# Kernel tuning notes

Measured on AMD Instinct MI355X. Metric: run time of the kernel, lower is better.

The kernel has to match this reference:

```python
import jax, jax.numpy as jnp
import numpy as np

WS = 8       # window size
NH = 8       # num heads


def _window_partition(x, ws):
    # x: [B, E, H, W] -> [B*Hn*Wn, ws*ws, E]
    B, E, H, W = x.shape
    Hn, Wn = H // ws, W // ws
    x = x.reshape(B, E, Hn, ws, Wn, ws)
    x = x.transpose(0, 2, 4, 3, 5, 1)  # B, Hn, Wn, ws1, ws2, E
    return x.reshape(B * Hn * Wn, ws * ws, E)


def _window_unpartition(x, B, H, W, ws):
    # x: [B*Hn*Wn, ws*ws, E] -> [B, E, H, W]
    Hn, Wn = H // ws, W // ws
    E = x.shape[-1]
    x = x.reshape(B, Hn, Wn, ws, ws, E)
    x = x.transpose(0, 5, 1, 3, 2, 4)  # B, E, Hn, ws1, Wn, ws2
    return x.reshape(B, E, H, W)


def setup_inputs() -> dict:
    key = jax.random.key(0)
    ks = jax.random.split(key, 5)
    B, E, H, W = 8, 512, 64, 64
    s = 1.0 / np.sqrt(E)
    return {
        "q": jax.random.normal(ks[0], (B, E, H, W), jnp.float32),
        "k": jax.random.normal(ks[1], (B, E, H, W), jnp.float32),
        "v": jax.random.normal(ks[2], (B, E, H, W), jnp.float32),
        "in_proj_w": (jax.random.normal(ks[3], (3 * E, E), jnp.float32) * s),
        "in_proj_b": jnp.zeros((3 * E,), jnp.float32),
        "out_proj_w": (jax.random.normal(ks[4], (E, E), jnp.float32) * s),
        "out_proj_b": jnp.zeros((E,), jnp.float32),
    }


def reference(q, k, v, in_proj_w, in_proj_b, out_proj_w, out_proj_b):
    B, E, H, W = q.shape
    ws, nh = WS, NH
    hd = E // nh

    qw = _window_partition(q, ws)  # [N, T, E], N = B*Hn*Wn, T = ws*ws
    kw = _window_partition(k, ws)
    vw = _window_partition(v, ws)

    Wq, Wk, Wv = in_proj_w[:E], in_proj_w[E:2 * E], in_proj_w[2 * E:]
    bq, bk, bv = in_proj_b[:E], in_proj_b[E:2 * E], in_proj_b[2 * E:]

    qp = qw @ Wq.T + bq
    kp = kw @ Wk.T + bk
    vp = vw @ Wv.T + bv

    N, T, _ = qp.shape
    qh = qp.reshape(N, T, nh, hd)
    kh = kp.reshape(N, T, nh, hd)
    vh = vp.reshape(N, T, nh, hd)

    scale = jnp.asarray(1.0 / np.sqrt(hd), qp.dtype)
    attn = jax.nn.softmax(jnp.einsum('nqhd,nkhd->nhqk', qh, kh) * scale, axis=-1)
    o = jnp.einsum('nhqk,nkhd->nqhd', attn, vh).reshape(N, T, E)
    o = o @ out_proj_w.T + out_proj_b

    return _window_unpartition(o, B, H, W, ws)
```

## Files before the change

kernel.cpp:

```cpp
#include <hip/hip_runtime.h>

typedef __attribute__((ext_vector_type(4))) float f32x4;
typedef __attribute__((ext_vector_type(8))) short short8;
typedef __attribute__((ext_vector_type(4))) unsigned uint4v;

#define E_DIM 512
#define HW    4096
#define NT    32768
#define NTE   16777216

__device__ short g_wbf[2048 * E_DIM];

__device__ __forceinline__ short f2bf(float f) {
  union { float f; unsigned u; } v; v.f = f;
  unsigned u = v.u;
  u += 0x7fffu + ((u >> 16) & 1u);
  return (short)(u >> 16);
}
__device__ __forceinline__ unsigned pack_bf2(float lo, float hi) {
  return (unsigned)(unsigned short)f2bf(lo) | ((unsigned)(unsigned short)f2bf(hi) << 16);
}

__device__ __forceinline__ int swzidx(int row, int k) {
  return row * 64 + (k ^ ((row & 7) << 3));
}

__device__ __forceinline__ void chunk_map(int c, int& row, int& kc) {
  const int line = c >> 3;
  const int l = (c & 7) ^ (line & 7);
  row = line * 2 + (l >> 2);
  kc = l & 3;
}
__device__ __forceinline__ int tile_off(int row, int kc) {
  const int line = row >> 1;
  const int phys = (((row & 1) << 2) | kc) ^ (line & 7);
  return line * 64 + phys * 8;
}

#define GLOAD16(g, l) __builtin_amdgcn_global_load_lds( \
    (const __attribute__((address_space(1))) void*)(g), \
    (__attribute__((address_space(3))) void*)(l), 16, 0, 0)

#define WAITVM(N) asm volatile("s_waitcnt vmcnt(" #N ")" ::: "memory")
#define LGKM0()   asm volatile("s_waitcnt lgkmcnt(0)" ::: "memory")
#define FULL_BAR() do { asm volatile("" ::: "memory"); \
  __builtin_amdgcn_s_barrier(); asm volatile("" ::: "memory"); } while (0)

__global__ __launch_bounds__(256) void convert_w(
    const float* __restrict__ w_in, const float* __restrict__ w_out)
{
  const size_t off = ((size_t)blockIdx.x * 256 + threadIdx.x) * 8;
  const float* src = (off < 786432) ? (w_in + off) : (w_out + (off - 786432));
  f32x4 a = *(const f32x4*)src, b = *(const f32x4*)(src + 4);
  short8 s;
#pragma unroll
  for (int j = 0; j < 4; ++j) { s[j] = f2bf(a[j]); s[4 + j] = f2bf(b[j]); }
  *(short8*)&g_wbf[off] = s;
}

__global__ __launch_bounds__(512, 2) void proj_kernel(
    const float* __restrict__ Xq, const float* __restrict__ Xk,
    const float* __restrict__ Xv, const float* __restrict__ Bfull,
    short* __restrict__ Oq, short* __restrict__ Ok, short* __restrict__ Ov)
{
  const int wg  = blockIdx.x;
  const int swz = (wg & 7) * 96 + (wg >> 3);
  const int z = swz >> 8, rr = swz & 255;
  const int e0 = (rr & 1) << 8, tok0 = (rr >> 1) << 8;

  const float* X  = (z == 0) ? Xq : (z == 1) ? Xk : Xv;
  const short* Wz = g_wbf + z * (E_DIM * E_DIM);
  const float* bias = Bfull + z * E_DIM;
  short* O = (z == 0) ? Oq : (z == 1) ? Ok : Ov;

  const int b   = tok0 >> 12;
  const int hw0 = tok0 & (HW - 1);
  const float* Xb = X + (size_t)b * E_DIM * HW + hw0;

  __shared__ unsigned ldsA[2 * 4096];
  __shared__ short    ldsB[3 * 8192];

  const int tid = threadIdx.x, lane = tid & 63, wv = tid >> 6;
  const int wm = wv >> 2, wn = wv & 3;
  const int lr = lane & 15, lg = lane >> 4;

  const int fp  = tid >> 5;
  const int hw8 = (tid & 31) * 8;
  const float* arow0 = Xb + (size_t)(2 * fp) * HW + hw8;
  const int keyw = (fp >> 3) << 4;
  const int aWbase = fp * 256 + (hw8 ^ keyw);

  int r0, k0c, r1, k1c;
  chunk_map(tid, r0, k0c);
  chunk_map(512 + tid, r1, k1c);
  const short* sB0 = Wz + (size_t)(e0 + r0) * E_DIM + k0c * 8;
  const short* sB1 = Wz + (size_t)(e0 + r1) * E_DIM + k1c * 8;
  const int dc0 = (wv * 64) * 8, dc1 = (512 + wv * 64) * 8;

  const int keyr = (lg >> 1) << 4;
  int aoff[8], boff[4];
#pragma unroll
  for (int i = 0; i < 8; ++i)
    aoff[i] = lg * 1024 + ((wm * 128 + i * 16 + lr) ^ keyr);
#pragma unroll
  for (int j = 0; j < 4; ++j) boff[j] = tile_off(wn * 64 + j * 16 + lr, lg);

  f32x4 acc[8][4];
#pragma unroll
  for (int i = 0; i < 8; ++i)
#pragma unroll
    for (int j = 0; j < 4; ++j) acc[i][j] = (f32x4){0.f, 0.f, 0.f, 0.f};

  f32x4 aX[4], aY[4];

#define ISSUE_A(dst, kt) do { \
    const float* ap = arow0 + (size_t)(kt) * (32 * HW); \
    dst[0] = *(const f32x4*)(ap);          dst[1] = *(const f32x4*)(ap + 4); \
    dst[2] = *(const f32x4*)(ap + HW);     dst[3] = *(const f32x4*)(ap + 4 + HW); \
  } while (0)

#define ISSUE_B(slot, kt) do { \
    const int ko2 = (kt) * 32, sb2 = (slot) * 8192; \
    GLOAD16(sB0 + ko2, &ldsB[sb2 + dc0]); \
    GLOAD16(sB1 + ko2, &ldsB[sb2 + dc1]); \
  } while (0)

#define WRITE_A(slot, src) do { \
    unsigned* dA = &ldsA[(slot) * 4096 + aWbase]; \
    uint4v lo_, hi_; \
    _Pragma("unroll") \
    for (int j = 0; j < 4; ++j) { \
      lo_[j] = pack_bf2(src[0][j], src[2][j]); \
      hi_[j] = pack_bf2(src[1][j], src[3][j]); \
    } \
    *(uint4v*)(dA) = lo_; \
    *(uint4v*)(dA + 4) = hi_; \
  } while (0)

#define COMPUTE(aslot, bslot) do { \
    const unsigned* pa = ldsA + (aslot) * 4096; \
    const short*    pb = ldsB + (bslot) * 8192; \
    short8 af[8], bf[4]; \
    _Pragma("unroll") \
    for (int i = 0; i < 8; ++i) { \
      union { unsigned u[4]; short8 s; } av_; \
      av_.u[0] = pa[aoff[i]];       av_.u[1] = pa[aoff[i] + 256]; \
      av_.u[2] = pa[aoff[i] + 512]; av_.u[3] = pa[aoff[i] + 768]; \
      af[i] = av_.s; \
    } \
    _Pragma("unroll") \
    for (int j = 0; j < 4; ++j) bf[j] = *(const short8*)(pb + boff[j]); \
    __builtin_amdgcn_s_setprio(1); \
    _Pragma("unroll") \
    for (int i = 0; i < 8; ++i) \
      _Pragma("unroll") \
      for (int j = 0; j < 4; ++j) \
        acc[i][j] = __builtin_amdgcn_mfma_f32_16x16x32_bf16(af[i], bf[j], acc[i][j], 0, 0, 0); \
    __builtin_amdgcn_s_setprio(0); \
  } while (0)

  ISSUE_B(0, 0); ISSUE_B(1, 1);
  ISSUE_A(aX, 0);
  ISSUE_A(aY, 1);
  WAITVM(4);
  WRITE_A(0, aX);

  ISSUE_A(aX, 2);
  WAITVM(4); LGKM0();
  FULL_BAR();
  ISSUE_B(2, 2);
  WRITE_A(1, aY);
  COMPUTE(0, 0);

  for (int k = 0; k < 6; ++k) {
    const int t = 2 * k + 1;
    ISSUE_A(aY, t + 2);
    WAITVM(6); LGKM0();
    FULL_BAR();
    ISSUE_B((t + 2) % 3, t + 2);
    WRITE_A(0, aX);
    COMPUTE(1, t % 3);
    ISSUE_A(aX, t + 3);
    WAITVM(6); LGKM0();
    FULL_BAR();
    ISSUE_B((t + 3) % 3, t + 3);
    WRITE_A(1, aY);
    COMPUTE(0, (t + 1) % 3);
  }

  ISSUE_A(aY, 15);
  WAITVM(6); LGKM0();
  FULL_BAR();
  ISSUE_B(0, 15);
  WRITE_A(0, aX);
  COMPUTE(1, 1);
  WAITVM(2); LGKM0();
  FULL_BAR();
  WRITE_A(1, aY);
  COMPUTE(0, 2);
  WAITVM(0); LGKM0();
  FULL_BAR();
  COMPUTE(1, 0);

#undef ISSUE_A
#undef ISSUE_B
#undef WRITE_A
#undef COMPUTE

  float bj[4];
#pragma unroll
  for (int j = 0; j < 4; ++j) bj[j] = bias[e0 + wn * 64 + j * 16 + lr];
#pragma unroll
  for (int i = 0; i < 8; ++i) {
#pragma unroll
    for (int r = 0; r < 4; ++r) {
      const int token = tok0 + wm * 128 + i * 16 + lg * 4 + r;
      const int hw = token & (HW - 1);
      const int h = hw >> 6, w = hw & 63;
      const int nwin = ((token >> 12) << 6) + ((h >> 3) << 3) + (w >> 3);
      const int twin = ((h & 7) << 3) + (w & 7);
      short* orow = O + ((size_t)(nwin * 64 + twin) << 9) + e0 + wn * 64 + lr;
#pragma unroll
      for (int j = 0; j < 4; ++j)
        orow[j * 16] = f2bf(acc[i][j][r] + bj[j]);
    }
  }
}

__global__ __launch_bounds__(256) void attn_kernel(
    const short* __restrict__ Qp, const short* __restrict__ Kp,
    const short* __restrict__ Vp, short* __restrict__ Ob)
{
  const int head = blockIdx.x, nwin = blockIdx.y;
  const int base = nwin * (64 * E_DIM) + head * 64;

  __shared__ short lQ[64 * 64];
  __shared__ short lK[64 * 64];
  __shared__ short lVT[64 * 64];

  const int tid = threadIdx.x;
  {
    const int row = tid >> 2, sg = (tid & 3) * 16;
    const int go = base + row * E_DIM + sg;
    *(short8*)&lQ[swzidx(row, sg)]     = *(const short8*)&Qp[go];
    *(short8*)&lQ[swzidx(row, sg + 8)] = *(const short8*)&Qp[go + 8];
    *(short8*)&lK[swzidx(row, sg)]     = *(const short8*)&Kp[go];
    *(short8*)&lK[swzidx(row, sg + 8)] = *(const short8*)&Kp[go + 8];
    const int tv = tid & 63, d0 = (tid >> 6) * 16;
    const int gv = base + tv * E_DIM + d0;
    short8 v0 = *(const short8*)&Vp[gv];
    short8 v1 = *(const short8*)&Vp[gv + 8];
#pragma unroll
    for (int ii = 0; ii < 8; ++ii) lVT[swzidx(d0 + ii, tv)] = v0[ii];
#pragma unroll
    for (int ii = 0; ii < 8; ++ii) lVT[swzidx(d0 + 8 + ii, tv)] = v1[ii];
  }
  __syncthreads();

  const int lane = tid & 63, wv = tid >> 6;
  const int lr = lane & 15, lg = lane >> 4;
  const int m0 = wv * 16;

  f32x4 s[4];
#pragma unroll
  for (int j = 0; j < 4; ++j) s[j] = (f32x4){0.f, 0.f, 0.f, 0.f};
#pragma unroll
  for (int ks = 0; ks < 2; ++ks) {
    const int kk = ks * 32 + lg * 8;
    short8 a = *(const short8*)&lQ[swzidx(m0 + lr, kk)];
#pragma unroll
    for (int j = 0; j < 4; ++j) {
      short8 b = *(const short8*)&lK[swzidx(j * 16 + lr, kk)];
      s[j] = __builtin_amdgcn_mfma_f32_16x16x32_bf16(a, b, s[j], 0, 0, 0);
    }
  }

  const float cexp = 0.125f * 1.4426950408889634f;
  float p[4][4], rs[4];
#pragma unroll
  for (int r = 0; r < 4; ++r) {
    float mx = fmaxf(fmaxf(s[0][r], s[1][r]), fmaxf(s[2][r], s[3][r]));
    mx = fmaxf(mx, __shfl_xor(mx, 1));
    mx = fmaxf(mx, __shfl_xor(mx, 2));
    mx = fmaxf(mx, __shfl_xor(mx, 4));
    mx = fmaxf(mx, __shfl_xor(mx, 8));
    float sm = 0.f;
#pragma unroll
    for (int j = 0; j < 4; ++j) { p[j][r] = exp2f((s[j][r] - mx) * cexp); sm += p[j][r]; }
    sm += __shfl_xor(sm, 1); sm += __shfl_xor(sm, 2);
    sm += __shfl_xor(sm, 4); sm += __shfl_xor(sm, 8);
    rs[r] = 1.0f / sm;
  }

#pragma unroll
  for (int r = 0; r < 4; ++r)
#pragma unroll
    for (int j = 0; j < 4; ++j)
      lQ[swzidx(m0 + lg * 4 + r, j * 16 + lr)] = f2bf(p[j][r]);

  f32x4 o[4];
#pragma unroll
  for (int nf = 0; nf < 4; ++nf) o[nf] = (f32x4){0.f, 0.f, 0.f, 0.f};
#pragma unroll
  for (int ks = 0; ks < 2; ++ks) {
    const int kk = ks * 32 + lg * 8;
    short8 a = *(const short8*)&lQ[swzidx(m0 + lr, kk)];
#pragma unroll
    for (int nf = 0; nf < 4; ++nf) {
      short8 b = *(const short8*)&lVT[swzidx(nf * 16 + lr, kk)];
      o[nf] = __builtin_amdgcn_mfma_f32_16x16x32_bf16(a, b, o[nf], 0, 0, 0);
    }
  }

#pragma unroll
  for (int r = 0; r < 4; ++r) {
    const int t = m0 + lg * 4 + r;
    short* orow = Ob + base + t * E_DIM + lr;
#pragma unroll
    for (int nf = 0; nf < 4; ++nf)
      orow[nf * 16] = f2bf(o[nf][r] * rs[r]);
  }
}

__global__ __launch_bounds__(512, 2) void oproj_kernel(
    const short* __restrict__ Ob, const float* __restrict__ bo,
    float* __restrict__ Out)
{
  const int wg  = blockIdx.x;
  const int swz = (wg & 7) * 32 + (wg >> 3);
  const int e0 = (swz & 1) << 8, tok0 = (swz >> 1) << 8;
  const short* Wo = g_wbf + 1536 * E_DIM;

  __shared__ short lds[4 * 16384];

  const int tid = threadIdx.x, lane = tid & 63, wv = tid >> 6;
  const int wm = wv >> 2, wn = wv & 3;
  const int lr = lane & 15, lg = lane >> 4;

  int r0, k0c, r1, k1c;
  chunk_map(tid, r0, k0c);
  chunk_map(512 + tid, r1, k1c);
  const short* sA0 = Wo + (size_t)(e0 + r0) * E_DIM + k0c * 8;
  const short* sA1 = Wo + (size_t)(e0 + r1) * E_DIM + k1c * 8;
  const short* sB0 = Ob + (size_t)(tok0 + r0) * E_DIM + k0c * 8;
  const short* sB1 = Ob + (size_t)(tok0 + r1) * E_DIM + k1c * 8;
  const int dc0 = (wv * 64) * 8, dc1 = (512 + wv * 64) * 8;

  int aoff[8], boff[4];
#pragma unroll
  for (int i = 0; i < 8; ++i) aoff[i] = tile_off(wm * 128 + i * 16 + lr, lg);
#pragma unroll
  for (int j = 0; j < 4; ++j) boff[j] = 8192 + tile_off(wn * 64 + j * 16 + lr, lg);

  f32x4 acc[8][4];
#pragma unroll
  for (int i = 0; i < 8; ++i)
#pragma unroll
    for (int j = 0; j < 4; ++j) acc[i][j] = (f32x4){0.f, 0.f, 0.f, 0.f};

  auto STAGE = [&](int slot, int kt) {
    const int sb = slot * 16384, ko = kt * 32;
    GLOAD16(sA0 + ko, &lds[sb + dc0]);
    GLOAD16(sA1 + ko, &lds[sb + dc1]);
    GLOAD16(sB0 + ko, &lds[sb + 8192 + dc0]);
    GLOAD16(sB1 + ko, &lds[sb + 8192 + dc1]);
  };
  auto COMPUTE = [&](int slot) {
    const int sb = slot * 16384;
    short8 af[8], bf[4];
#pragma unroll
    for (int i = 0; i < 8; ++i) af[i] = *(const short8*)&lds[sb + aoff[i]];
#pragma unroll
    for (int j = 0; j < 4; ++j) bf[j] = *(const short8*)&lds[sb + boff[j]];
    __builtin_amdgcn_s_setprio(1);
#pragma unroll
    for (int i = 0; i < 8; ++i)
#pragma unroll
      for (int j = 0; j < 4; ++j)
        acc[i][j] = __builtin_amdgcn_mfma_f32_16x16x32_bf16(af[i], bf[j], acc[i][j], 0, 0, 0);
    __builtin_amdgcn_s_setprio(0);
  };

  STAGE(0, 0); STAGE(1, 1); STAGE(2, 2);
  for (int t = 0; t < 13; ++t) {
    WAITVM(8);
    FULL_BAR();
    STAGE((t + 3) & 3, t + 3);
    COMPUTE(t & 3);
  }
  WAITVM(8); FULL_BAR(); COMPUTE(13 & 3);
  WAITVM(4); FULL_BAR(); COMPUTE(14 & 3);
  WAITVM(0); FULL_BAR(); COMPUTE(15 & 3);

#pragma unroll
  for (int i = 0; i < 8; ++i) {
#pragma unroll
    for (int r = 0; r < 4; ++r) {
      const int e = e0 + wm * 128 + i * 16 + lg * 4 + r;
      const float be = bo[e];
#pragma unroll
      for (int j = 0; j < 4; ++j) {
        const int wtok = tok0 + wn * 64 + j * 16 + lr;
        const int n = wtok >> 6, t = wtok & 63;
        const int b = n >> 6;
        const int h = (((n >> 3) & 7) << 3) + (t >> 3);
        const int w = ((n & 7) << 3) + (t & 7);
        Out[(size_t)b * (E_DIM * HW) + (size_t)e * HW + (h << 6) + w] =
            acc[i][j][r] + be;
      }
    }
  }
}

extern "C" void kernel_launch(void* const* d_in, const int* in_sizes, int n_in,
                              void* d_out, int out_size, void* d_ws, size_t ws_size,
                              hipStream_t stream) {
  const float* q     = (const float*)d_in[0];
  const float* k     = (const float*)d_in[1];
  const float* v     = (const float*)d_in[2];
  const float* in_w  = (const float*)d_in[3];
  const float* in_b  = (const float*)d_in[4];
  const float* out_w = (const float*)d_in[5];
  const float* out_b = (const float*)d_in[6];
  float* out = (float*)d_out;

  short* qp = (short*)d_ws;
  short* kp = qp + NTE;
  short* vp = kp + NTE;
  short* ob = vp + NTE;

  convert_w<<<512, 256, 0, stream>>>(in_w, out_w);
  proj_kernel<<<768, 512, 0, stream>>>(q, k, v, in_b, qp, kp, vp);
  attn_kernel<<<dim3(8, 512), 256, 0, stream>>>(qp, kp, vp, ob);
  oproj_kernel<<<256, 512, 0, stream>>>(ob, out_b, out);
}
```

Measured before the change: 161.4 us.

## Triple-buffer A register prefetch and re-swizzle A LDS layout in projection GEMM

The QKV projection GEMM now keeps three register buffers of fp32 A tiles in flight instead of two, so global loads are issued one stage further ahead. The bf16 conversion and LDS write of the next A tile move inside the compute macro, after the fragment reads, so they overlap with the MFMA work. The A LDS swizzle changes to 8-byte stores with an XOR key, and the fragment reads change to match, aimed at reducing bank conflicts on both writes and reads. This costs more VGPRs for the extra prefetch buffer, which may lower occupancy, and the hand-unrolled schedule is harder to verify.

After: 246.0 us (median of 3 runs). 52.4% more time.

```diff
diff --git a/kernel.cpp b/kernel.cpp
--- a/kernel.cpp
+++ b/kernel.cpp
@@ -2,7 +2,7 @@
 
 typedef __attribute__((ext_vector_type(4))) float f32x4;
 typedef __attribute__((ext_vector_type(8))) short short8;
-typedef __attribute__((ext_vector_type(4))) unsigned uint4v;
+typedef __attribute__((ext_vector_type(2))) unsigned uint2v;
 
 #define E_DIM 512
 #define HW    4096
@@ -84,11 +84,11 @@
   const int wm = wv >> 2, wn = wv & 3;
   const int lr = lane & 15, lg = lane >> 4;
 
-  const int fp  = tid >> 5;
-  const int hw8 = (tid & 31) * 8;
-  const float* arow0 = Xb + (size_t)(2 * fp) * HW + hw8;
-  const int keyw = (fp >> 3) << 4;
-  const int aWbase = fp * 256 + (hw8 ^ keyw);
+  const int fp = tid >> 5;
+  const int m  = tid & 31;
+  const float* arow0 = Xb + (size_t)(2 * fp) * HW + m * 8;
+  const int awbase = fp * 256 + ((m * 8) ^ ((fp >> 3) << 4));
+  const int wkey   = ((m >> 2) & 3) ^ ((fp & 1) << 1);
 
   int r0, k0c, r1, k1c;
   chunk_map(tid, r0, k0c);
@@ -97,21 +97,23 @@
   const short* sB1 = Wz + (size_t)(e0 + r1) * E_DIM + k1c * 8;
   const int dc0 = (wv * 64) * 8, dc1 = (512 + wv * 64) * 8;
 
-  const int keyr = (lg >> 1) << 4;
-  int aoff[8], boff[4];
+  int abase[8], boff[4];
+#pragma unroll
+  for (int i = 0; i < 8; ++i) {
+    const int T = wm * 128 + i * 16 + lr;
+    abase[i] = lg * 1024 + ((T & ~7) ^ ((lg >> 1) << 4))
+             + ((((T >> 1) & 3) ^ ((T >> 5) & 3)) << 1) + (T & 1);
+  }
+#pragma unroll
+  for (int j = 0; j < 4; ++j) boff[j] = tile_off(wn * 64 + j * 16 + lr, lg);
+
+  f32x4 acc[8][4];
 #pragma unroll
   for (int i = 0; i < 8; ++i)
-    aoff[i] = lg * 1024 + ((wm * 128 + i * 16 + lr) ^ keyr);
-#pragma unroll
-  for (int j = 0; j < 4; ++j) boff[j] = tile_off(wn * 64 + j * 16 + lr, lg);
-
-  f32x4 acc[8][4];
-#pragma unroll
-  for (int i = 0; i < 8; ++i)
 #pragma unroll
     for (int j = 0; j < 4; ++j) acc[i][j] = (f32x4){0.f, 0.f, 0.f, 0.f};
 
-  f32x4 aX[4], aY[4];
+  f32x4 aR0[4], aR1[4], aR2[4];
 
 #define ISSUE_A(dst, kt) do { \
     const float* ap = arow0 + (size_t)(kt) * (32 * HW); \
@@ -126,30 +128,32 @@
   } while (0)
 
 #define WRITE_A(slot, src) do { \
-    unsigned* dA = &ldsA[(slot) * 4096 + aWbase]; \
-    uint4v lo_, hi_; \
-    _Pragma("unroll") \
-    for (int j = 0; j < 4; ++j) { \
-      lo_[j] = pack_bf2(src[0][j], src[2][j]); \
-      hi_[j] = pack_bf2(src[1][j], src[3][j]); \
+    unsigned* dA = &ldsA[(slot) * 4096 + awbase]; \
+    _Pragma("unroll") \
+    for (int c2 = 0; c2 < 4; ++c2) { \
+      uint2v p_; \
+      p_[0] = pack_bf2(src[(2*c2) >> 2][(2*c2) & 3],     src[2 + ((2*c2) >> 2)][(2*c2) & 3]); \
+      p_[1] = pack_bf2(src[(2*c2+1) >> 2][(2*c2+1) & 3], src[2 + ((2*c2+1) >> 2)][(2*c2+1) & 3]); \
+      *(uint2v*)(dA + ((c2 ^ wkey) << 1)) = p_; \
     } \
-    *(uint4v*)(dA) = lo_; \
-    *(uint4v*)(dA + 4) = hi_; \
-  } while (0)
-
-#define COMPUTE(aslot, bslot) do { \
+  } while (0)
+
+#define COMPUTE2(aslot, bslot, wslot, wreg) do { \
     const unsigned* pa = ldsA + (aslot) * 4096; \
     const short*    pb = ldsB + (bslot) * 8192; \
     short8 af[8], bf[4]; \
     _Pragma("unroll") \
     for (int i = 0; i < 8; ++i) { \
       union { unsigned u[4]; short8 s; } av_; \
-      av_.u[0] = pa[aoff[i]];       av_.u[1] = pa[aoff[i] + 256]; \
-      av_.u[2] = pa[aoff[i] + 512]; av_.u[3] = pa[aoff[i] + 768]; \
+      av_.u[0] = pa[abase[i]]; \
+      av_.u[1] = pa[(abase[i] ^ 4) + 256]; \
+      av_.u[2] = pa[abase[i] + 512]; \
+      av_.u[3] = pa[(abase[i] ^ 4) + 768]; \
       af[i] = av_.s; \
     } \
     _Pragma("unroll") \
     for (int j = 0; j < 4; ++j) bf[j] = *(const short8*)(pb + boff[j]); \
+    WRITE_A(wslot, wreg); \
     __builtin_amdgcn_s_setprio(1); \
     _Pragma("unroll") \
     for (int i = 0; i < 8; ++i) \
@@ -159,53 +163,79 @@
     __builtin_amdgcn_s_setprio(0); \
   } while (0)
 
+#define COMPUTE1(aslot, bslot) do { \
+    const unsigned* pa = ldsA + (aslot) * 4096; \
+    const short*    pb = ldsB + (bslot) * 8192; \
+    short8 af[8], bf[4]; \
+    _Pragma("unroll") \
+    for (int i = 0; i < 8; ++i) { \
+      union { unsigned u[4]; short8 s; } av_; \
+      av_.u[0] = pa[abase[i]]; \
+      av_.u[1] = pa[(abase[i] ^ 4) + 256]; \
+      av_.u[2] = pa[abase[i] + 512]; \
+      av_.u[3] = pa[(abase[i] ^ 4) + 768]; \
+      af[i] = av_.s; \
+    } \
+    _Pragma("unroll") \
+    for (int j = 0; j < 4; ++j) bf[j] = *(const short8*)(pb + boff[j]); \
+    __builtin_amdgcn_s_setprio(1); \
+    _Pragma("unroll") \
+    for (int i = 0; i < 8; ++i) \
+      _Pragma("unroll") \
+      for (int j = 0; j < 4; ++j) \
+        acc[i][j] = __builtin_amdgcn_mfma_f32_16x16x32_bf16(af[i], bf[j], acc[i][j], 0, 0, 0); \
+    __builtin_amdgcn_s_setprio(0); \
+  } while (0)
+
+#define STEP(T, RI, RW, AC, AW, BS, BI) do { \
+    ISSUE_A(RI, (T) + 3); \
+    WAITVM(10); LGKM0(); \
+    FULL_BAR(); \
+    ISSUE_B(BI, (T) + 2); \
+    COMPUTE2(AC, BS, AW, RW); \
+  } while (0)
+
   ISSUE_B(0, 0); ISSUE_B(1, 1);
-  ISSUE_A(aX, 0);
-  ISSUE_A(aY, 1);
-  WAITVM(4);
-  WRITE_A(0, aX);
-
-  ISSUE_A(aX, 2);
-  WAITVM(4); LGKM0();
+  ISSUE_A(aR0, 0); ISSUE_A(aR1, 1); ISSUE_A(aR2, 2);
+  WAITVM(8);
+  WRITE_A(0, aR0);
+
+  ISSUE_A(aR0, 3);
+  WAITVM(8); LGKM0();
   FULL_BAR();
   ISSUE_B(2, 2);
-  WRITE_A(1, aY);
-  COMPUTE(0, 0);
-
-  for (int k = 0; k < 6; ++k) {
-    const int t = 2 * k + 1;
-    ISSUE_A(aY, t + 2);
-    WAITVM(6); LGKM0();
-    FULL_BAR();
-    ISSUE_B((t + 2) % 3, t + 2);
-    WRITE_A(0, aX);
-    COMPUTE(1, t % 3);
-    ISSUE_A(aX, t + 3);
-    WAITVM(6); LGKM0();
-    FULL_BAR();
-    ISSUE_B((t + 3) % 3, t + 3);
-    WRITE_A(1, aY);
-    COMPUTE(0, (t + 1) % 3);
-  }
-
-  ISSUE_A(aY, 15);
+  COMPUTE2(0, 0, 1, aR1);
+
+  STEP(1,  aR1, aR2, 1, 0, 1, 0);
+  STEP(2,  aR2, aR0, 0, 1, 2, 1);
+  STEP(3,  aR0, aR1, 1, 0, 0, 2);
+  STEP(4,  aR1, aR2, 0, 1, 1, 0);
+  STEP(5,  aR2, aR0, 1, 0, 2, 1);
+  STEP(6,  aR0, aR1, 0, 1, 0, 2);
+  STEP(7,  aR1, aR2, 1, 0, 1, 0);
+  STEP(8,  aR2, aR0, 0, 1, 2, 1);
+  STEP(9,  aR0, aR1, 1, 0, 0, 2);
+  STEP(10, aR1, aR2, 0, 1, 1, 0);
+  STEP(11, aR2, aR0, 1, 0, 2, 1);
+  STEP(12, aR0, aR1, 0, 1, 0, 2);
+
   WAITVM(6); LGKM0();
   FULL_BAR();
   ISSUE_B(0, 15);
-  WRITE_A(0, aX);
-  COMPUTE(1, 1);
+  COMPUTE2(1, 1, 0, aR2);
   WAITVM(2); LGKM0();
   FULL_BAR();
-  WRITE_A(1, aY);
-  COMPUTE(0, 2);
+  COMPUTE2(0, 2, 1, aR0);
   WAITVM(0); LGKM0();
   FULL_BAR();
-  COMPUTE(1, 0);
+  COMPUTE1(1, 0);
 
 #undef ISSUE_A
 #undef ISSUE_B
 #undef WRITE_A
-#undef COMPUTE
+#undef COMPUTE2
+#undef COMPUTE1
+#undef STEP
 
   float bj[4];
 #pragma unroll
```

## Fuse window attention and output projection into one per-window kernel

Applied to the files above, without the earlier changes.

Replaces the separate attention kernel and the tiled output-projection GEMM with a single kernel that handles one window per block, one head per wave. The attention output stays in LDS as bf16 and is multiplied by Wo straight from global memory, which removes the Ob round-trip through HBM and one launch. In exchange, each block reloads the full 512x512 Wo from L2 with no LDS staging or software pipelining. The grid shrinks to 512 blocks with 128KB of LDS each, which limits occupancy.

New measurement: 196.5 us. +21.8%, slower.

```diff
diff --git a/kernel.cpp b/kernel.cpp
--- a/kernel.cpp
+++ b/kernel.cpp
@@ -19,10 +19,6 @@
 }
 __device__ __forceinline__ unsigned pack_bf2(float lo, float hi) {
   return (unsigned)(unsigned short)f2bf(lo) | ((unsigned)(unsigned short)f2bf(hi) << 16);
-}
-
-__device__ __forceinline__ int swzidx(int row, int k) {
-  return row * 64 + (k ^ ((row & 7) << 3));
 }
 
 __device__ __forceinline__ void chunk_map(int c, int& row, int& kc) {
@@ -84,7 +80,7 @@
   const int wm = wv >> 2, wn = wv & 3;
   const int lr = lane & 15, lg = lane >> 4;
 
-  const int fp  = tid >> 5;
+  const int fp = tid >> 5;
   const int hw8 = (tid & 31) * 8;
   const float* arow0 = Xb + (size_t)(2 * fp) * HW + hw8;
   const int keyw = (fp >> 3) << 4;
@@ -159,7 +155,8 @@
     __builtin_amdgcn_s_setprio(0); \
   } while (0)
 
-  ISSUE_B(0, 0); ISSUE_B(1, 1);
+  ISSUE_B(0, 0);
+  ISSUE_B(1, 1);
   ISSUE_A(aX, 0);
   ISSUE_A(aY, 1);
   WAITVM(4);
@@ -227,189 +224,160 @@
   }
 }
 
-__global__ __launch_bounds__(256) void attn_kernel(
+__global__ __launch_bounds__(512) void attn_oproj(
     const short* __restrict__ Qp, const short* __restrict__ Kp,
-    const short* __restrict__ Vp, short* __restrict__ Ob)
-{
-  const int head = blockIdx.x, nwin = blockIdx.y;
-  const int base = nwin * (64 * E_DIM) + head * 64;
-
-  __shared__ short lQ[64 * 64];
-  __shared__ short lK[64 * 64];
-  __shared__ short lVT[64 * 64];
-
-  const int tid = threadIdx.x;
-  {
-    const int row = tid >> 2, sg = (tid & 3) * 16;
-    const int go = base + row * E_DIM + sg;
-    *(short8*)&lQ[swzidx(row, sg)]     = *(const short8*)&Qp[go];
-    *(short8*)&lQ[swzidx(row, sg + 8)] = *(const short8*)&Qp[go + 8];
-    *(short8*)&lK[swzidx(row, sg)]     = *(const short8*)&Kp[go];
-    *(short8*)&lK[swzidx(row, sg + 8)] = *(const short8*)&Kp[go + 8];
-    const int tv = tid & 63, d0 = (tid >> 6) * 16;
-    const int gv = base + tv * E_DIM + d0;
-    short8 v0 = *(const short8*)&Vp[gv];
-    short8 v1 = *(const short8*)&Vp[gv + 8];
-#pragma unroll
-    for (int ii = 0; ii < 8; ++ii) lVT[swzidx(d0 + ii, tv)] = v0[ii];
-#pragma unroll
-    for (int ii = 0; ii < 8; ++ii) lVT[swzidx(d0 + 8 + ii, tv)] = v1[ii];
-  }
-  __syncthreads();
-
-  const int lane = tid & 63, wv = tid >> 6;
-  const int lr = lane & 15, lg = lane >> 4;
-  const int m0 = wv * 16;
-
-  f32x4 s[4];
-#pragma unroll
-  for (int j = 0; j < 4; ++j) s[j] = (f32x4){0.f, 0.f, 0.f, 0.f};
-#pragma unroll
-  for (int ks = 0; ks < 2; ++ks) {
-    const int kk = ks * 32 + lg * 8;
-    short8 a = *(const short8*)&lQ[swzidx(m0 + lr, kk)];
-#pragma unroll
-    for (int j = 0; j < 4; ++j) {
-      short8 b = *(const short8*)&lK[swzidx(j * 16 + lr, kk)];
-      s[j] = __builtin_amdgcn_mfma_f32_16x16x32_bf16(a, b, s[j], 0, 0, 0);
-    }
-  }
-
-  const float cexp = 0.125f * 1.4426950408889634f;
-  float p[4][4], rs[4];
-#pragma unroll
-  for (int r = 0; r < 4; ++r) {
-    float mx = fmaxf(fmaxf(s[0][r], s[1][r]), fmaxf(s[2][r], s[3][r]));
-    mx = fmaxf(mx, __shfl_xor(mx, 1));
-    mx = fmaxf(mx, __shfl_xor(mx, 2));
-    mx = fmaxf(mx, __shfl_xor(mx, 4));
-    mx = fmaxf(mx, __shfl_xor(mx, 8));
-    float sm = 0.f;
-#pragma unroll
-    for (int j = 0; j < 4; ++j) { p[j][r] = exp2f((s[j][r] - mx) * cexp); sm += p[j][r]; }
-    sm += __shfl_xor(sm, 1); sm += __shfl_xor(sm, 2);
-    sm += __shfl_xor(sm, 4); sm += __shfl_xor(sm, 8);
-    rs[r] = 1.0f / sm;
-  }
-
-#pragma unroll
-  for (int r = 0; r < 4; ++r)
-#pragma unroll
-    for (int j = 0; j < 4; ++j)
-      lQ[swzidx(m0 + lg * 4 + r, j * 16 + lr)] = f2bf(p[j][r]);
-
-  f32x4 o[4];
-#pragma unroll
-  for (int nf = 0; nf < 4; ++nf) o[nf] = (f32x4){0.f, 0.f, 0.f, 0.f};
-#pragma unroll
-  for (int ks = 0; ks < 2; ++ks) {
-    const int kk = ks * 32 + lg * 8;
-    short8 a = *(const short8*)&lQ[swzidx(m0 + lr, kk)];
-#pragma unroll
-    for (int nf = 0; nf < 4; ++nf) {
-      short8 b = *(const short8*)&lVT[swzidx(nf * 16 + lr, kk)];
-      o[nf] = __builtin_amdgcn_mfma_f32_16x16x32_bf16(a, b, o[nf], 0, 0, 0);
-    }
-  }
-
-#pragma unroll
-  for (int r = 0; r < 4; ++r) {
-    const int t = m0 + lg * 4 + r;
-    short* orow = Ob + base + t * E_DIM + lr;
-#pragma unroll
-    for (int nf = 0; nf < 4; ++nf)
-      orow[nf * 16] = f2bf(o[nf][r] * rs[r]);
-  }
-}
-
-__global__ __launch_bounds__(512, 2) void oproj_kernel(
-    const short* __restrict__ Ob, const float* __restrict__ bo,
+    const short* __restrict__ Vp, const float* __restrict__ bo,
     float* __restrict__ Out)
 {
-  const int wg  = blockIdx.x;
-  const int swz = (wg & 7) * 32 + (wg >> 3);
-  const int e0 = (swz & 1) << 8, tok0 = (swz >> 1) << 8;
+  const int nwin = blockIdx.x;
+  const int tid = threadIdx.x, lane = tid & 63, h = tid >> 6;
+  const int lr = lane & 15, lg = lane >> 4;
+  const size_t base = (size_t)nwin * (64 * E_DIM) + h * 64;
+
+  __shared__ short R1[64 * 512];
+  __shared__ short R2[64 * 512];
+  short* P  = R1 + h * 4096;
+  short* VT = R2 + h * 4096;
+
+  short8 q8[4][2];
+#pragma unroll
+  for (int i = 0; i < 4; ++i)
+#pragma unroll
+    for (int ks = 0; ks < 2; ++ks)
+      q8[i][ks] = *(const short8*)&Qp[base + (size_t)(i * 16 + lr) * E_DIM + ks * 32 + lg * 8];
+
+  {
+    const int vr = lane >> 3, vc = lane & 7;
+#pragma unroll
+    for (int r8 = 0; r8 < 8; ++r8) {
+      const int row = r8 * 8 + vr;
+      short8 v8 = *(const short8*)&Vp[base + (size_t)row * E_DIM + vc * 8];
+#pragma unroll
+      for (int ii = 0; ii < 8; ++ii) {
+        const int d = vc * 8 + ii;
+        VT[d * 64 + (row ^ ((((d & 7) ^ (d >> 3)) & 7) << 3))] = v8[ii];
+      }
+    }
+  }
+
+  f32x4 s[4][4];
+#pragma unroll
+  for (int i = 0; i < 4; ++i)
+#pragma unroll
+    for (int j = 0; j < 4; ++j) s[i][j] = (f32x4){0.f, 0.f, 0.f, 0.f};
+#pragma unroll
+  for (int ks = 0; ks < 2; ++ks)
+#pragma unroll
+    for (int j = 0; j < 4; ++j) {
+      short8 k8 = *(const short8*)&Kp[base + (size_t)(j * 16 + lr) * E_DIM + ks * 32 + lg * 8];
+#pragma unroll
+      for (int i = 0; i < 4; ++i)
+        s[i][j] = __builtin_amdgcn_mfma_f32_16x16x32_bf16(q8[i][ks], k8, s[i][j], 0, 0, 0);
+    }
+
+  const float cexp = 0.125f * 1.4426950408889634f;
+  float rs[4][4];
+#pragma unroll
+  for (int i = 0; i < 4; ++i)
+#pragma unroll
+    for (int r = 0; r < 4; ++r) {
+      float mx = fmaxf(fmaxf(s[i][0][r], s[i][1][r]), fmaxf(s[i][2][r], s[i][3][r]));
+      mx = fmaxf(mx, __shfl_xor(mx, 1));
+      mx = fmaxf(mx, __shfl_xor(mx, 2));
+      mx = fmaxf(mx, __shfl_xor(mx, 4));
+      mx = fmaxf(mx, __shfl_xor(mx, 8));
+      float p[4], sm = 0.f;
+#pragma unroll
+      for (int j = 0; j < 4; ++j) { p[j] = exp2f((s[i][j][r] - mx) * cexp); sm += p[j]; }
+      sm += __shfl_xor(sm, 1); sm += __shfl_xor(sm, 2);
+      sm += __shfl_xor(sm, 4); sm += __shfl_xor(sm, 8);
+      rs[i][r] = 1.0f / sm;
+      const int t = i * 16 + lg * 4 + r;
+#pragma unroll
+      for (int j = 0; j < 4; ++j)
+        P[t * 64 + ((j * 16 + lr) ^ ((t & 7) << 3))] = f2bf(p[j]);
+    }
+
+  f32x4 o[4][4];
+#pragma unroll
+  for (int i = 0; i < 4; ++i)
+#pragma unroll
+    for (int nf = 0; nf < 4; ++nf) o[i][nf] = (f32x4){0.f, 0.f, 0.f, 0.f};
+#pragma unroll
+  for (int ks = 0; ks < 2; ++ks) {
+    short8 vt8[4];
+#pragma unroll
+    for (int nf = 0; nf < 4; ++nf) {
+      const int d = nf * 16 + lr;
+      vt8[nf] = *(const short8*)&VT[d * 64 + ((ks * 32 + lg * 8) ^ ((((d & 7) ^ (d >> 3)) & 7) << 3))];
+    }
+#pragma unroll
+    for (int i = 0; i < 4; ++i) {
+      const int t = i * 16 + lr;
+      short8 pa8 = *(const short8*)&P[t * 64 + ((ks * 32 + lg * 8) ^ ((t & 7) << 3))];
+#pragma unroll
+      for (int nf = 0; nf < 4; ++nf)
+        o[i][nf] = __builtin_amdgcn_mfma_f32_16x16x32_bf16(pa8, vt8[nf], o[i][nf], 0, 0, 0);
+    }
+  }
+
+  __syncthreads();
+
+#pragma unroll
+  for (int i = 0; i < 4; ++i)
+#pragma unroll
+    for (int r = 0; r < 4; ++r) {
+      const int t = i * 16 + lg * 4 + r;
+      const int swzk = (t & 7) << 3;
+#pragma unroll
+      for (int nf = 0; nf < 4; ++nf)
+        R1[t * 512 + ((h * 64 + nf * 16 + lr) ^ swzk)] = f2bf(o[i][nf][r] * rs[i][r]);
+    }
+
+  __syncthreads();
+
   const short* Wo = g_wbf + 1536 * E_DIM;
-
-  __shared__ short lds[4 * 16384];
-
-  const int tid = threadIdx.x, lane = tid & 63, wv = tid >> 6;
-  const int wm = wv >> 2, wn = wv & 3;
-  const int lr = lane & 15, lg = lane >> 4;
-
-  int r0, k0c, r1, k1c;
-  chunk_map(tid, r0, k0c);
-  chunk_map(512 + tid, r1, k1c);
-  const short* sA0 = Wo + (size_t)(e0 + r0) * E_DIM + k0c * 8;
-  const short* sA1 = Wo + (size_t)(e0 + r1) * E_DIM + k1c * 8;
-  const short* sB0 = Ob + (size_t)(tok0 + r0) * E_DIM + k0c * 8;
-  const short* sB1 = Ob + (size_t)(tok0 + r1) * E_DIM + k1c * 8;
-  const int dc0 = (wv * 64) * 8, dc1 = (512 + wv * 64) * 8;
-
-  int aoff[8], boff[4];
-#pragma unroll
-  for (int i = 0; i < 8; ++i) aoff[i] = tile_off(wm * 128 + i * 16 + lr, lg);
-#pragma unroll
-  for (int j = 0; j < 4; ++j) boff[j] = 8192 + tile_off(wn * 64 + j * 16 + lr, lg);
-
-  f32x4 acc[8][4];
-#pragma unroll
-  for (int i = 0; i < 8; ++i)
-#pragma unroll
-    for (int j = 0; j < 4; ++j) acc[i][j] = (f32x4){0.f, 0.f, 0.f, 0.f};
-
-  auto STAGE = [&](int slot, int kt) {
-    const int sb = slot * 16384, ko = kt * 32;
-    GLOAD16(sA0 + ko, &lds[sb + dc0]);
-    GLOAD16(sA1 + ko, &lds[sb + dc1]);
-    GLOAD16(sB0 + ko, &lds[sb + 8192 + dc0]);
-    GLOAD16(sB1 + ko, &lds[sb + 8192 + dc1]);
-  };
-  auto COMPUTE = [&](int slot) {
-    const int sb = slot * 16384;
-    short8 af[8], bf[4];
-#pragma unroll
-    for (int i = 0; i < 8; ++i) af[i] = *(const short8*)&lds[sb + aoff[i]];
-#pragma unroll
-    for (int j = 0; j < 4; ++j) bf[j] = *(const short8*)&lds[sb + boff[j]];
-    __builtin_amdgcn_s_setprio(1);
-#pragma unroll
-    for (int i = 0; i < 8; ++i)
-#pragma unroll
-      for (int j = 0; j < 4; ++j)
-        acc[i][j] = __builtin_amdgcn_mfma_f32_16x16x32_bf16(af[i], bf[j], acc[i][j], 0, 0, 0);
-    __builtin_amdgcn_s_setprio(0);
-  };
-
-  STAGE(0, 0); STAGE(1, 1); STAGE(2, 2);
-  for (int t = 0; t < 13; ++t) {
-    WAITVM(8);
-    FULL_BAR();
-    STAGE((t + 3) & 3, t + 3);
-    COMPUTE(t & 3);
+  const int E0 = h * 64;
+  f32x4 o2[4][4];
+#pragma unroll
+  for (int mi = 0; mi < 4; ++mi)
+#pragma unroll
+    for (int nj = 0; nj < 4; ++nj) o2[mi][nj] = (f32x4){0.f, 0.f, 0.f, 0.f};
+
+#pragma unroll 2
+  for (int k0 = 0; k0 < E_DIM; k0 += 32) {
+    short8 wa[4], ob8[4];
+#pragma unroll
+    for (int mi = 0; mi < 4; ++mi)
+      wa[mi] = *(const short8*)&Wo[(size_t)(E0 + mi * 16 + lr) * E_DIM + k0 + lg * 8];
+#pragma unroll
+    for (int nj = 0; nj < 4; ++nj) {
+      const int t = nj * 16 + lr;
+      ob8[nj] = *(const short8*)&R1[t * 512 + ((k0 + lg * 8) ^ ((t & 7) << 3))];
+    }
+#pragma unroll
+    for (int mi = 0; mi < 4; ++mi)
+#pragma unroll
+      for (int nj = 0; nj < 4; ++nj)
+        o2[mi][nj] = __builtin_amdgcn_mfma_f32_16x16x32_bf16(wa[mi], ob8[nj], o2[mi][nj], 0, 0, 0);
   }
-  WAITVM(8); FULL_BAR(); COMPUTE(13 & 3);
-  WAITVM(4); FULL_BAR(); COMPUTE(14 & 3);
-  WAITVM(0); FULL_BAR(); COMPUTE(15 & 3);
-
-#pragma unroll
-  for (int i = 0; i < 8; ++i) {
+
+  const int bb = nwin >> 6;
+  const int wh0 = ((nwin >> 3) & 7) << 3, ww0 = (nwin & 7) << 3;
+  float* outb = Out + (size_t)bb * (E_DIM * HW);
+#pragma unroll
+  for (int mi = 0; mi < 4; ++mi)
 #pragma unroll
     for (int r = 0; r < 4; ++r) {
-      const int e = e0 + wm * 128 + i * 16 + lg * 4 + r;
+      const int e = E0 + mi * 16 + lg * 4 + r;
       const float be = bo[e];
 #pragma unroll
-      for (int j = 0; j < 4; ++j) {
-        const int wtok = tok0 + wn * 64 + j * 16 + lr;
-        const int n = wtok >> 6, t = wtok & 63;
-        const int b = n >> 6;
-        const int h = (((n >> 3) & 7) << 3) + (t >> 3);
-        const int w = ((n & 7) << 3) + (t & 7);
-        Out[(size_t)b * (E_DIM * HW) + (size_t)e * HW + (h << 6) + w] =
-            acc[i][j][r] + be;
+      for (int nj = 0; nj < 4; ++nj) {
+        const int t = nj * 16 + lr;
+        outb[(size_t)e * HW + (wh0 + (t >> 3)) * 64 + ww0 + (t & 7)] =
+            o2[mi][nj][r] + be;
       }
     }
-  }
 }
 
 extern "C" void kernel_launch(void* const* d_in, const int* in_sizes, int n_in,
@@ -427,10 +395,8 @@
   short* qp = (short*)d_ws;
   short* kp = qp + NTE;
   short* vp = kp + NTE;
-  short* ob = vp + NTE;
 
   convert_w<<<512, 256, 0, stream>>>(in_w, out_w);
   proj_kernel<<<768, 512, 0, stream>>>(q, k, v, in_b, qp, kp, vp);
-  attn_kernel<<<dim3(8, 512), 256, 0, stream>>>(qp, kp, vp, ob);
-  oproj_kernel<<<256, 512, 0, stream>>>(ob, out_b, out);
-}
+  attn_oproj<<<512, 512, 0, stream>>>(qp, kp, vp, out_b, out);
+}
```
